# Kernel tuning notes

Measured on AMD Instinct MI355X. Metric: run time of the kernel, lower is better.

The kernel has to match this reference:

```python
import jax, jax.numpy as jnp
import numpy as np

B, T, H, NH = 16, 2048, 1024, 16
HD = H // NH  # 64
IN0, IN1 = 256, 512  # modality input sizes needing projection; modality 2 is already H


def _ln(x, g, b, eps=1e-5):
    m = jnp.mean(x, axis=-1, keepdims=True)
    v = jnp.mean((x - m) ** 2, axis=-1, keepdims=True)
    return (x - m) / jnp.sqrt(v + eps) * g + b


def setup_inputs() -> dict:
    key = jax.random.key(0)
    ks = jax.random.split(key, 24)
    s = 0.02
    d = {
        'x0': jax.random.normal(ks[0], (B, T, IN0), jnp.float32),
        'x1': jax.random.normal(ks[1], (B, T, IN1), jnp.float32),
        'x2': jax.random.normal(ks[2], (B, T, H), jnp.float32),
        'static_context': jax.random.normal(ks[3], (B, T, H), jnp.float32),
        'Wp0': jax.random.normal(ks[4], (H, IN0), jnp.float32) * s,
        'bp0': jnp.zeros((H,), jnp.float32),
        'Wp1': jax.random.normal(ks[5], (H, IN1), jnp.float32) * s,
        'bp1': jnp.zeros((H,), jnp.float32),
        'Wq': jax.random.normal(ks[6], (H, H), jnp.float32) * s,
        'bq': jnp.zeros((H,), jnp.float32),
        'Wk': jax.random.normal(ks[7], (H, H), jnp.float32) * s,
        'bk': jnp.zeros((H,), jnp.float32),
        'Wv': jax.random.normal(ks[8], (H, H), jnp.float32) * s,
        'bv': jnp.zeros((H,), jnp.float32),
        'Wo': jax.random.normal(ks[9], (H, H), jnp.float32) * s,
        'bo': jnp.zeros((H,), jnp.float32),
        'query_token': jax.random.normal(ks[10], (H,), jnp.float32) * s,
        'g1': jnp.ones((H,), jnp.float32),
        'be1': jnp.zeros((H,), jnp.float32),
        'g2': jnp.ones((H,), jnp.float32),
        'be2': jnp.zeros((H,), jnp.float32),
        'W1': jax.random.normal(ks[11], (4 * H, H), jnp.float32) * s,
        'b1': jnp.zeros((4 * H,), jnp.float32),
        'W2': jax.random.normal(ks[12], (H, 4 * H), jnp.float32) * s,
        'b2': jnp.zeros((H,), jnp.float32),
    }
    return d


def _forward(x0, x1, x2, static_context, Wp0, bp0, Wp1, bp1, Wq, bq, Wk, bk, Wv, bv,
             Wo, bo, query_token, g1, be1, g2, be2, W1, b1, W2, b2):
    # project modalities to hidden size, stack -> [B, T, M, H]
    m0 = x0 @ Wp0.T + bp0
    m1 = x1 @ Wp1.T + bp1
    stacked = jnp.stack([m0, m1, x2], axis=2)  # [B,T,3,H]
    M = stacked.shape[2]
    # per-timestep single-query cross-attention over the M modality tokens,
    # batched over all B*T positions (equivalent to the torch per-t loop)
    q = query_token + static_context  # [B,T,H]
    Q = (q @ Wq.T + bq).reshape(B, T, NH, HD)
    K = (stacked @ Wk.T + bk).reshape(B, T, M, NH, HD)
    V = (stacked @ Wv.T + bv).reshape(B, T, M, NH, HD)
    scores = jnp.einsum('bthd,btmhd->bthm', Q, K) / jnp.sqrt(jnp.asarray(HD, Q.dtype))
    attn = jax.nn.softmax(scores, axis=-1)  # [B,T,NH,M]
    weights = attn.mean(axis=2)  # average over heads (torch default) -> [B,T,M]
    ctx = jnp.einsum('bthm,btmhd->bthd', attn, V).reshape(B, T, H)
    attn_out = ctx @ Wo.T + bo
    fused = _ln(attn_out, g1, be1)
    ff = jax.nn.gelu(fused @ W1.T + b1, approximate=False) @ W2.T + b2
    fused = _ln(fused + ff, g2, be2)
    return fused, weights


def reference(x0, x1, x2, static_context, Wp0, bp0, Wp1, bp1, Wq, bq, Wk, bk, Wv, bv,
              Wo, bo, query_token, g1, be1, g2, be2, W1, b1, W2, b2):
    return _forward(x0, x1, x2, static_context, Wp0, bp0, Wp1, bp1, Wq, bq, Wk, bk,
                    Wv, bv, Wo, bo, query_token, g1, be1, g2, be2, W1, b1, W2, b2)
```

## Files before the change

### kernel.cpp

```cpp
#include <hip/hip_runtime.h>
#include <hip/hip_bf16.h>
#include <math.h>

#define BT 32768
#define HH 1024

typedef unsigned short u16;
typedef __attribute__((ext_vector_type(4))) unsigned short u16x4;
typedef __attribute__((ext_vector_type(8))) unsigned short u16x8;
typedef __attribute__((ext_vector_type(8))) __bf16 bf16x8;
typedef __attribute__((ext_vector_type(4))) float f32x4;

#define DEVI static __device__ __forceinline__

DEVI u16 f2bf(float f){
  unsigned u = __builtin_bit_cast(unsigned, f);
  u += 0x7FFFu + ((u >> 16) & 1u);
  return (u16)(u >> 16);
}
DEVI float bf2f(u16 h){
  unsigned u = ((unsigned)h) << 16;
  return __builtin_bit_cast(float, u);
}
DEVI void gl_lds16(const void* g, void* l){
  __builtin_amdgcn_global_load_lds((const __attribute__((address_space(1))) void*)g,
                                   (__attribute__((address_space(3))) void*)l, 16, 0, 0);
}
DEVI int swz(int row, int elem){ return elem ^ ((row & 7) << 3); }

__global__ void k_cast4(const float* __restrict__ s, u16* __restrict__ d, int n4){
  int i = blockIdx.x*blockDim.x + threadIdx.x;
  int st = gridDim.x*blockDim.x;
  for (; i < n4; i += st){
    float4 v = ((const float4*)s)[i];
    u16x4 o = { f2bf(v.x), f2bf(v.y), f2bf(v.z), f2bf(v.w) };
    ((u16x4*)d)[i] = o;
  }
}

__global__ void k_qb(const float* __restrict__ qt, const float* __restrict__ sc,
                     u16* __restrict__ d, int n4){
  int i = blockIdx.x*blockDim.x + threadIdx.x;
  int st = gridDim.x*blockDim.x;
  for (; i < n4; i += st){
    int e = i*4; int c = e & 1023;
    float4 v = *(const float4*)&sc[e];
    float4 q = *(const float4*)&qt[c];
    u16x4 o = { f2bf(v.x+q.x), f2bf(v.y+q.y), f2bf(v.z+q.z), f2bf(v.w+q.w) };
    ((u16x4*)d)[i] = o;
  }
}

__global__ void k_copyf(const float* __restrict__ s, float* __restrict__ d, int n){
  int i = blockIdx.x*blockDim.x + threadIdx.x;
  int st = gridDim.x*blockDim.x;
  for (; i < n; i += st) d[i] = s[i];
}

__global__ void k_wmean(const float* __restrict__ p, float* __restrict__ out, int n){
  int i = blockIdx.x*blockDim.x + threadIdx.x;
  int st = gridDim.x*blockDim.x;
  for (; i < n; i += st){
    int t = i/3, m = i - t*3;
    float s = 0.f;
    #pragma unroll
    for (int h = 0; h < 16; ++h) s += p[(size_t)t*48 + h*3 + m];
    out[i] = s * 0.0625f;
  }
}

__global__ void k_transcast(const float* __restrict__ s, u16* __restrict__ d, int R, int C){
  __shared__ float tile[32][33];
  int c0 = blockIdx.x*32, r0 = blockIdx.y*32;
  int tx = threadIdx.x & 31, ty = threadIdx.x >> 5;
  #pragma unroll
  for (int i = 0; i < 32; i += 8) tile[ty+i][tx] = s[(size_t)(r0+ty+i)*C + c0+tx];
  __syncthreads();
  #pragma unroll
  for (int i = 0; i < 32; i += 8) d[(size_t)(c0+ty+i)*R + r0+tx] = f2bf(tile[tx][ty+i]);
}

__global__ void k_matvec(const u16* __restrict__ W, const float* __restrict__ x,
                         const float* __restrict__ badd, float* __restrict__ out, int K){
  int row = blockIdx.x*4 + (threadIdx.x>>6);
  int lane = threadIdx.x & 63;
  float s = 0.f;
  for (int k = lane; k < K; k += 64) s += bf2f(W[(size_t)row*K + k]) * x[k];
  #pragma unroll
  for (int m = 1; m < 64; m <<= 1) s += __shfl_xor(s, m);
  if (lane == 0) out[row] = s + badd[row];
}

__global__ __launch_bounds__(256, 3)
void k_gemm(const u16* __restrict__ A, int lda,
            const u16* __restrict__ B, int ldb, int K,
            const float* __restrict__ bias,
            u16* __restrict__ C, int ldc, int col0, int act)
{
  __shared__ u16 As[128*64];
  __shared__ u16 Bs[128*64];
  const int tid = threadIdx.x, lane = tid & 63, wid = tid >> 6;
  const int wr = wid >> 1, wc = wid & 1;
  const int r15 = lane & 15, g = lane >> 4;
  const int m0 = blockIdx.x * 128, n0 = blockIdx.y * 128;
  f32x4 acc[4][4] = {};

  for (int k0 = 0; k0 < K; k0 += 64){
    #pragma unroll
    for (int it = 0; it < 4; ++it){
      int c = it*256 + tid;
      int row = c >> 3;
      int ke = swz(row, (c & 7) * 8);
      gl_lds16(A + (size_t)(m0+row)*lda + (k0+ke), As + c*8);
      gl_lds16(B + (size_t)(n0+row)*ldb + (k0+ke), Bs + c*8);
    }
    __syncthreads();
    #pragma unroll
    for (int kk = 0; kk < 64; kk += 32){
      bf16x8 av[4], bvv[4];
      #pragma unroll
      for (int i = 0; i < 4; ++i){
        int row = wr*64 + i*16 + r15;
        av[i] = *(const bf16x8*)&As[row*64 + swz(row, kk + g*8)];
      }
      #pragma unroll
      for (int j = 0; j < 4; ++j){
        int row = wc*64 + j*16 + r15;
        bvv[j] = *(const bf16x8*)&Bs[row*64 + swz(row, kk + g*8)];
      }
      #pragma unroll
      for (int i = 0; i < 4; ++i)
        #pragma unroll
        for (int j = 0; j < 4; ++j)
          acc[i][j] = __builtin_amdgcn_mfma_f32_16x16x32_bf16(av[i], bvv[j], acc[i][j], 0, 0, 0);
    }
    __syncthreads();
  }
  #pragma unroll
  for (int j = 0; j < 4; ++j){
    int col = wc*64 + j*16 + r15;
    float bb = bias ? bias[n0 + col] : 0.f;
    #pragma unroll
    for (int i = 0; i < 4; ++i){
      #pragma unroll
      for (int jj = 0; jj < 4; ++jj){
        int row = wr*64 + i*16 + g*4 + jj;
        float v = acc[i][j][jj] + bb;
        if (act == 1) v = 0.5f * v * (1.f + erff(v * 0.70710678118654752f));
        C[(size_t)(m0+row)*ldc + col0 + n0 + col] = f2bf(v);
      }
    }
  }
}

__global__ __launch_bounds__(256, 2)
void k_attnf(const u16* __restrict__ x0b, const u16* __restrict__ x1b, const u16* __restrict__ x2b,
             const u16* __restrict__ Wc0, const u16* __restrict__ Wc1, const u16* __restrict__ Wc2,
             const float* __restrict__ bc0, const float* __restrict__ bc1, const float* __restrict__ bc2,
             const u16* __restrict__ Qg, u16* __restrict__ ctx, float* __restrict__ pbuf)
{
  __shared__ u16 As[128*64];
  __shared__ u16 Bs[128*64];
  __shared__ float Sl[2*128*3];
  const int tid = threadIdx.x, lane = tid & 63, wid = tid >> 6;
  const int wr = wid >> 1, wc = wid & 1;
  const int r15 = lane & 15, g = lane >> 4;
  const int bid = blockIdx.x;
  const int xcd = bid & 7, bn = (bid >> 3) & 7, btb = (bid >> 6) * 8 + xcd;
  const int t0 = btb * 128, n0 = bn * 128;

  const u16* Xs[3] = { x0b, x1b, x2b };
  const u16* Ws[3] = { Wc0, Wc1, Wc2 };
  const float* Bc[3] = { bc0, bc1, bc2 };
  const int Ks[3] = { 256, 512, 1024 };

  float qreg[4][4][4];
  #pragma unroll
  for (int i = 0; i < 4; ++i)
    #pragma unroll
    for (int jj = 0; jj < 4; ++jj){
      int row = wr*64 + i*16 + g*4 + jj;
      const u16* qr = Qg + (size_t)(t0+row)*1024 + n0 + wc*64 + r15;
      #pragma unroll
      for (int j = 0; j < 4; ++j) qreg[i][jj][j] = bf2f(qr[j*16]);
    }

  #pragma unroll
  for (int m = 0; m < 3; ++m){
    const int K = Ks[m];
    const u16* X = Xs[m];
    const u16* W = Ws[m];
    f32x4 acc[4][4] = {};
    for (int k0 = 0; k0 < K; k0 += 64){
      #pragma unroll
      for (int it = 0; it < 4; ++it){
        int c = it*256 + tid;
        int row = c >> 3;
        int ke = swz(row, (c & 7) * 8);
        gl_lds16(X + (size_t)(t0+row)*K + (k0+ke), As + c*8);
        gl_lds16(W + (size_t)(n0+row)*K + (k0+ke), Bs + c*8);
      }
      __syncthreads();
      #pragma unroll
      for (int kk = 0; kk < 64; kk += 32){
        bf16x8 av[4], bvv[4];
        #pragma unroll
        for (int i = 0; i < 4; ++i){
          int row = wr*64 + i*16 + r15;
          av[i] = *(const bf16x8*)&As[row*64 + swz(row, kk + g*8)];
        }
        #pragma unroll
        for (int j = 0; j < 4; ++j){
          int row = wc*64 + j*16 + r15;
          bvv[j] = *(const bf16x8*)&Bs[row*64 + swz(row, kk + g*8)];
        }
        #pragma unroll
        for (int i = 0; i < 4; ++i)
          #pragma unroll
          for (int j = 0; j < 4; ++j)
            acc[i][j] = __builtin_amdgcn_mfma_f32_16x16x32_bf16(av[i], bvv[j], acc[i][j], 0, 0, 0);
      }
      __syncthreads();
    }
    float bkc[4];
    #pragma unroll
    for (int j = 0; j < 4; ++j) bkc[j] = Bc[m][n0 + wc*64 + j*16 + r15];
    #pragma unroll
    for (int i = 0; i < 4; ++i){
      #pragma unroll
      for (int jj = 0; jj < 4; ++jj){
        int row = wr*64 + i*16 + g*4 + jj;
        float sv = 0.f;
        #pragma unroll
        for (int j = 0; j < 4; ++j)
          sv += (acc[i][j][jj] + bkc[j]) * qreg[i][jj][j];
        sv += __shfl_xor(sv, 1); sv += __shfl_xor(sv, 2);
        sv += __shfl_xor(sv, 4); sv += __shfl_xor(sv, 8);
        if (r15 == 0) Sl[(wc*128 + row)*3 + m] = sv * 0.125f;
      }
    }
  }
  __syncthreads();

  {
    int h2 = tid >> 7, tt = tid & 127;
    int base = (h2*128 + tt)*3;
    float s0 = Sl[base+0], s1 = Sl[base+1], s2 = Sl[base+2];
    float mx = fmaxf(s0, fmaxf(s1, s2));
    float e0 = __expf(s0-mx), e1 = __expf(s1-mx), e2 = __expf(s2-mx);
    float inv = 1.f/(e0+e1+e2);
    e0 *= inv; e1 *= inv; e2 *= inv;
    __syncthreads();
    Sl[base+0] = e0; Sl[base+1] = e1; Sl[base+2] = e2;
    float* pp = pbuf + ((size_t)(t0+tt)*16 + (bn*2 + h2))*3;
    pp[0] = e0; pp[1] = e1; pp[2] = e2;
  }
  __syncthreads();

  f32x4 cx[4][4] = {};
  #pragma unroll
  for (int m = 0; m < 3; ++m){
    const int K = Ks[m];
    const u16* X = Xs[m];
    const u16* W = Ws[m] + (size_t)1024*K;
    f32x4 acc[4][4] = {};
    for (int k0 = 0; k0 < K; k0 += 64){
      #pragma unroll
      for (int it = 0; it < 4; ++it){
        int c = it*256 + tid;
        int row = c >> 3;
        int ke = swz(row, (c & 7) * 8);
        gl_lds16(X + (size_t)(t0+row)*K + (k0+ke), As + c*8);
        gl_lds16(W + (size_t)(n0+row)*K + (k0+ke), Bs + c*8);
      }
      __syncthreads();
      #pragma unroll
      for (int kk = 0; kk < 64; kk += 32){
        bf16x8 av[4], bvv[4];
        #pragma unroll
        for (int i = 0; i < 4; ++i){
          int row = wr*64 + i*16 + r15;
          av[i] = *(const bf16x8*)&As[row*64 + swz(row, kk + g*8)];
        }
        #pragma unroll
        for (int j = 0; j < 4; ++j){
          int row = wc*64 + j*16 + r15;
          bvv[j] = *(const bf16x8*)&Bs[row*64 + swz(row, kk + g*8)];
        }
        #pragma unroll
        for (int i = 0; i < 4; ++i)
          #pragma unroll
          for (int j = 0; j < 4; ++j)
            acc[i][j] = __builtin_amdgcn_mfma_f32_16x16x32_bf16(av[i], bvv[j], acc[i][j], 0, 0, 0);
      }
      __syncthreads();
    }
    float bvc[4];
    #pragma unroll
    for (int j = 0; j < 4; ++j) bvc[j] = Bc[m][1024 + n0 + wc*64 + j*16 + r15];
    #pragma unroll
    for (int i = 0; i < 4; ++i){
      #pragma unroll
      for (int jj = 0; jj < 4; ++jj){
        int row = wr*64 + i*16 + g*4 + jj;
        float p = Sl[(wc*128 + row)*3 + m];
        #pragma unroll
        for (int j = 0; j < 4; ++j)
          cx[i][j][jj] += p * (acc[i][j][jj] + bvc[j]);
      }
    }
  }
  #pragma unroll
  for (int i = 0; i < 4; ++i){
    #pragma unroll
    for (int jj = 0; jj < 4; ++jj){
      int row = wr*64 + i*16 + g*4 + jj;
      #pragma unroll
      for (int j = 0; j < 4; ++j)
        ctx[(size_t)(t0+row)*1024 + n0 + wc*64 + j*16 + r15] = f2bf(cx[i][j][jj]);
    }
  }
}

__global__ __launch_bounds__(256)
void k_ln(const u16* __restrict__ X, const u16* __restrict__ R,
          const float* __restrict__ gam, const float* __restrict__ bet,
          u16* __restrict__ outb, float* __restrict__ outf)
{
  __shared__ float rs[4], rq[4];
  const int t = blockIdx.x, tid = threadIdx.x;
  const size_t base = (size_t)t*1024 + tid*4;
  u16x4 xv = *(const u16x4*)&X[base];
  float v[4];
  #pragma unroll
  for (int i = 0; i < 4; ++i) v[i] = bf2f(xv[i]);
  if (R){
    u16x4 rv = *(const u16x4*)&R[base];
    #pragma unroll
    for (int i = 0; i < 4; ++i) v[i] += bf2f(rv[i]);
  }
  float s = v[0]+v[1]+v[2]+v[3];
  float q = v[0]*v[0]+v[1]*v[1]+v[2]*v[2]+v[3]*v[3];
  #pragma unroll
  for (int m = 1; m < 64; m <<= 1){ s += __shfl_xor(s, m); q += __shfl_xor(q, m); }
  if ((tid & 63) == 0){ rs[tid>>6] = s; rq[tid>>6] = q; }
  __syncthreads();
  s = rs[0]+rs[1]+rs[2]+rs[3];
  q = rq[0]+rq[1]+rq[2]+rq[3];
  float mean = s * (1.f/1024.f);
  float var  = q * (1.f/1024.f) - mean*mean;
  float rstd = rsqrtf(var + 1e-5f);
  int c0 = tid*4;
  if (outb){
    u16x4 o;
    #pragma unroll
    for (int i = 0; i < 4; ++i) o[i] = f2bf((v[i]-mean)*rstd*gam[c0+i] + bet[c0+i]);
    *(u16x4*)&outb[base] = o;
  } else {
    float4 o;
    o.x = (v[0]-mean)*rstd*gam[c0+0] + bet[c0+0];
    o.y = (v[1]-mean)*rstd*gam[c0+1] + bet[c0+1];
    o.z = (v[2]-mean)*rstd*gam[c0+2] + bet[c0+2];
    o.w = (v[3]-mean)*rstd*gam[c0+3] + bet[c0+3];
    *(float4*)&outf[base] = o;
  }
}

extern "C" void kernel_launch(void* const* d_in, const int* in_sizes, int n_in,
                              void* d_out, int out_size, void* d_ws, size_t ws_size,
                              hipStream_t stream)
{
  (void)in_sizes; (void)n_in; (void)out_size;
  const float* x0  = (const float*)d_in[0];
  const float* x1  = (const float*)d_in[1];
  const float* x2  = (const float*)d_in[2];
  const float* sc  = (const float*)d_in[3];
  const float* Wp0 = (const float*)d_in[4];  const float* bp0 = (const float*)d_in[5];
  const float* Wp1 = (const float*)d_in[6];  const float* bp1 = (const float*)d_in[7];
  const float* Wq  = (const float*)d_in[8];  const float* bq  = (const float*)d_in[9];
  const float* Wk  = (const float*)d_in[10]; const float* bk  = (const float*)d_in[11];
  const float* Wv  = (const float*)d_in[12]; const float* bv  = (const float*)d_in[13];
  const float* Wo  = (const float*)d_in[14]; const float* bo  = (const float*)d_in[15];
  const float* qt  = (const float*)d_in[16];
  const float* g1  = (const float*)d_in[17]; const float* be1 = (const float*)d_in[18];
  const float* g2  = (const float*)d_in[19]; const float* be2 = (const float*)d_in[20];
  const float* W1  = (const float*)d_in[21]; const float* b1  = (const float*)d_in[22];
  const float* W2  = (const float*)d_in[23]; const float* b2  = (const float*)d_in[24];

  char* ws = (char*)d_ws;
  size_t off = 0;
  auto alloc = [&](size_t b)->char*{ char* p = ws + off; off += (b + 255) & ~(size_t)255; return p; };

  u16* Wqb   = (u16*)alloc((size_t)1024*1024*2);
  u16* Wob   = (u16*)alloc((size_t)1024*1024*2);
  u16* W1b   = (u16*)alloc((size_t)4096*1024*2);
  u16* W2b   = (u16*)alloc((size_t)1024*4096*2);
  u16* Wkvb  = (u16*)alloc((size_t)2048*1024*2);
  u16* Wp0t  = (u16*)alloc((size_t)256*1024*2);
  u16* Wp1t  = (u16*)alloc((size_t)512*1024*2);
  u16* Wkv0c = (u16*)alloc((size_t)2048*256*2);
  u16* Wkv1c = (u16*)alloc((size_t)2048*512*2);
  float* bc0 = (float*)alloc((size_t)2048*4);
  float* bc1 = (float*)alloc((size_t)2048*4);
  float* bc2 = (float*)alloc((size_t)2048*4);
  char* regX  = alloc((size_t)BT*(256+512+1024)*2);
  char* regQ1 = alloc((size_t)BT*1024*2);
  char* regQ2 = alloc((size_t)BT*1024*2);
  float* pbuf = (float*)alloc((size_t)BT*48*4);
  if (off > ws_size) return;

  u16* x0b = (u16*)regX;
  u16* x1b = (u16*)(regX + (size_t)BT*256*2);
  u16* x2b = (u16*)(regX + (size_t)BT*768*2);
  u16* aob  = (u16*)regX;
  u16* ff2b = (u16*)regX;
  u16* qb   = (u16*)regQ1;
  u16* ctxb = (u16*)regQ1;
  u16* f1b  = (u16*)regQ1;
  u16* Qb   = (u16*)regQ2;
  u16* ff1c = (u16*)regQ2;

  dim3 B256(256);
  auto cast4 = [&](const float* s, u16* d, int n, int grid){
    k_cast4<<<dim3(grid), B256, 0, stream>>>(s, d, n >> 2);
  };
  cast4(Wq, Wqb, 1024*1024, 1024);
  cast4(Wk, Wkvb, 1024*1024, 1024);
  cast4(Wv, Wkvb + (size_t)1024*1024, 1024*1024, 1024);
  cast4(Wo, Wob, 1024*1024, 1024);
  cast4(W1, W1b, 4096*1024, 1024);
  cast4(W2, W2b, 4096*1024, 1024);
  cast4(x0, x0b, BT*256, 1024);
  cast4(x1, x1b, BT*512, 1024);
  cast4(x2, x2b, BT*1024, 2048);
  k_transcast<<<dim3(8, 32),  B256, 0, stream>>>(Wp0, Wp0t, 1024, 256);
  k_transcast<<<dim3(16, 32), B256, 0, stream>>>(Wp1, Wp1t, 1024, 512);
  k_copyf<<<dim3(4), B256, 0, stream>>>(bk, bc2, 1024);
  k_copyf<<<dim3(4), B256, 0, stream>>>(bv, bc2 + 1024, 1024);
  k_matvec<<<dim3(512), B256, 0, stream>>>(Wkvb, bp0, bc2, bc0, 1024);
  k_matvec<<<dim3(512), B256, 0, stream>>>(Wkvb, bp1, bc2, bc1, 1024);
  k_qb<<<dim3(2048), B256, 0, stream>>>(qt, sc, qb, BT*256);

  k_gemm<<<dim3(16, 2), B256, 0, stream>>>(Wkvb, 1024, Wp0t, 1024, 1024, nullptr, Wkv0c, 256, 0, 0);
  k_gemm<<<dim3(16, 4), B256, 0, stream>>>(Wkvb, 1024, Wp1t, 1024, 1024, nullptr, Wkv1c, 512, 0, 0);

  k_gemm<<<dim3(BT/128, 8), B256, 0, stream>>>(qb, 1024, Wqb, 1024, 1024, bq, Qb, 1024, 0, 0);
  k_attnf<<<dim3(BT/128*8), B256, 0, stream>>>(x0b, x1b, x2b, Wkv0c, Wkv1c, Wkvb,
                                               bc0, bc1, bc2, Qb, ctxb, pbuf);
  float* outf = (float*)d_out;
  k_wmean<<<dim3(384), B256, 0, stream>>>(pbuf, outf + (size_t)BT*1024, BT*3);
  k_gemm<<<dim3(BT/128, 8), B256, 0, stream>>>(ctxb, 1024, Wob, 1024, 1024, bo, aob, 1024, 0, 0);
  k_ln<<<dim3(BT), B256, 0, stream>>>(aob, nullptr, g1, be1, f1b, nullptr);

  for (int c = 0; c < 4; ++c){
    const u16* fa = f1b + (size_t)c*8192*1024;
    k_gemm<<<dim3(64, 32), B256, 0, stream>>>(fa, 1024, W1b, 1024, 1024, b1, ff1c, 4096, 0, 1);
    k_gemm<<<dim3(64, 8),  B256, 0, stream>>>(ff1c, 4096, W2b, 4096, 4096, b2,
                                              ff2b + (size_t)c*8192*1024, 1024, 0, 0);
  }
  k_ln<<<dim3(BT), B256, 0, stream>>>(ff2b, f1b, g2, be2, nullptr, outf);
}
```

Baseline: 1.549 ms.

## Cut register pressure in fused attention kernel to raise occupancy

The Q values are no longer held in 64 registers per thread; they are staged through LDS after each K projection. The separate per-modality context accumulator is removed: a single V accumulator is rescaled by ratios of the softmax probabilities between modalities, and biases are applied at the end. Together these free registers, and the launch bound goes from 2 to 3 blocks per SIMD. The risks are extra LDS traffic and barriers, and the probability ratios need a floor clamp to avoid dividing by zero, which changes the rounding behaviour.

```diff
diff --git a/kernel.cpp b/kernel.cpp
--- a/kernel.cpp
+++ b/kernel.cpp
@@ -6,6 +6,7 @@
 #define HH 1024
 
 typedef unsigned short u16;
+typedef unsigned int u32;
 typedef __attribute__((ext_vector_type(4))) unsigned short u16x4;
 typedef __attribute__((ext_vector_type(8))) unsigned short u16x8;
 typedef __attribute__((ext_vector_type(8))) __bf16 bf16x8;
@@ -153,7 +154,7 @@
   }
 }
 
-__global__ __launch_bounds__(256, 2)
+__global__ __launch_bounds__(256, 3)
 void k_attnf(const u16* __restrict__ x0b, const u16* __restrict__ x1b, const u16* __restrict__ x2b,
              const u16* __restrict__ Wc0, const u16* __restrict__ Wc1, const u16* __restrict__ Wc2,
              const float* __restrict__ bc0, const float* __restrict__ bc1, const float* __restrict__ bc2,
@@ -174,17 +175,6 @@
   const float* Bc[3] = { bc0, bc1, bc2 };
   const int Ks[3] = { 256, 512, 1024 };
 
-  float qreg[4][4][4];
-  #pragma unroll
-  for (int i = 0; i < 4; ++i)
-    #pragma unroll
-    for (int jj = 0; jj < 4; ++jj){
-      int row = wr*64 + i*16 + g*4 + jj;
-      const u16* qr = Qg + (size_t)(t0+row)*1024 + n0 + wc*64 + r15;
-      #pragma unroll
-      for (int j = 0; j < 4; ++j) qreg[i][jj][j] = bf2f(qr[j*16]);
-    }
-
   #pragma unroll
   for (int m = 0; m < 3; ++m){
     const int K = Ks[m];
@@ -222,6 +212,16 @@
       }
       __syncthreads();
     }
+    #pragma unroll
+    for (int it = 0; it < 4; ++it){
+      int c = it*256 + tid;
+      int row = c >> 3;
+      int ke = swz(row, (c & 7) * 8);
+      gl_lds16(Qg + (size_t)(t0+row)*1024 + n0 + ke,      As + c*8);
+      gl_lds16(Qg + (size_t)(t0+row)*1024 + n0 + 64 + ke, Bs + c*8);
+    }
+    __syncthreads();
+    const u16* QL = wc ? Bs : As;
     float bkc[4];
     #pragma unroll
     for (int j = 0; j < 4; ++j) bkc[j] = Bc[m][n0 + wc*64 + j*16 + r15];
@@ -233,14 +233,14 @@
         float sv = 0.f;
         #pragma unroll
         for (int j = 0; j < 4; ++j)
-          sv += (acc[i][j][jj] + bkc[j]) * qreg[i][jj][j];
+          sv += (acc[i][j][jj] + bkc[j]) * bf2f(QL[row*64 + swz(row, j*16 + r15)]);
         sv += __shfl_xor(sv, 1); sv += __shfl_xor(sv, 2);
         sv += __shfl_xor(sv, 4); sv += __shfl_xor(sv, 8);
         if (r15 == 0) Sl[(wc*128 + row)*3 + m] = sv * 0.125f;
       }
     }
-  }
-  __syncthreads();
+    __syncthreads();
+  }
 
   {
     int h2 = tid >> 7, tt = tid & 127;
@@ -249,7 +249,7 @@
     float mx = fmaxf(s0, fmaxf(s1, s2));
     float e0 = __expf(s0-mx), e1 = __expf(s1-mx), e2 = __expf(s2-mx);
     float inv = 1.f/(e0+e1+e2);
-    e0 *= inv; e1 *= inv; e2 *= inv;
+    e0 = fmaxf(e0*inv, 1e-30f); e1 = fmaxf(e1*inv, 1e-30f); e2 = fmaxf(e2*inv, 1e-30f);
     __syncthreads();
     Sl[base+0] = e0; Sl[base+1] = e1; Sl[base+2] = e2;
     float* pp = pbuf + ((size_t)(t0+tt)*16 + (bn*2 + h2))*3;
@@ -257,67 +257,77 @@
   }
   __syncthreads();
 
-  f32x4 cx[4][4] = {};
-  #pragma unroll
-  for (int m = 0; m < 3; ++m){
-    const int K = Ks[m];
-    const u16* X = Xs[m];
-    const u16* W = Ws[m] + (size_t)1024*K;
+  {
     f32x4 acc[4][4] = {};
-    for (int k0 = 0; k0 < K; k0 += 64){
-      #pragma unroll
-      for (int it = 0; it < 4; ++it){
-        int c = it*256 + tid;
-        int row = c >> 3;
-        int ke = swz(row, (c & 7) * 8);
-        gl_lds16(X + (size_t)(t0+row)*K + (k0+ke), As + c*8);
-        gl_lds16(W + (size_t)(n0+row)*K + (k0+ke), Bs + c*8);
-      }
-      __syncthreads();
-      #pragma unroll
-      for (int kk = 0; kk < 64; kk += 32){
-        bf16x8 av[4], bvv[4];
+    #pragma unroll
+    for (int m = 0; m < 3; ++m){
+      const int K = Ks[m];
+      const u16* X = Xs[m];
+      const u16* W = Ws[m] + (size_t)1024*K;
+      if (m > 0){
         #pragma unroll
         for (int i = 0; i < 4; ++i){
-          int row = wr*64 + i*16 + r15;
-          av[i] = *(const bf16x8*)&As[row*64 + swz(row, kk + g*8)];
-        }
-        #pragma unroll
-        for (int j = 0; j < 4; ++j){
-          int row = wc*64 + j*16 + r15;
-          bvv[j] = *(const bf16x8*)&Bs[row*64 + swz(row, kk + g*8)];
-        }
-        #pragma unroll
-        for (int i = 0; i < 4; ++i)
           #pragma unroll
-          for (int j = 0; j < 4; ++j)
-            acc[i][j] = __builtin_amdgcn_mfma_f32_16x16x32_bf16(av[i], bvv[j], acc[i][j], 0, 0, 0);
-      }
-      __syncthreads();
-    }
-    float bvc[4];
-    #pragma unroll
-    for (int j = 0; j < 4; ++j) bvc[j] = Bc[m][1024 + n0 + wc*64 + j*16 + r15];
+          for (int jj = 0; jj < 4; ++jj){
+            int row = wr*64 + i*16 + g*4 + jj;
+            float r = Sl[(wc*128+row)*3 + (m-1)] / Sl[(wc*128+row)*3 + m];
+            #pragma unroll
+            for (int j = 0; j < 4; ++j) acc[i][j][jj] *= r;
+          }
+        }
+      }
+      for (int k0 = 0; k0 < K; k0 += 64){
+        #pragma unroll
+        for (int it = 0; it < 4; ++it){
+          int c = it*256 + tid;
+          int row = c >> 3;
+          int ke = swz(row, (c & 7) * 8);
+          gl_lds16(X + (size_t)(t0+row)*K + (k0+ke), As + c*8);
+          gl_lds16(W + (size_t)(n0+row)*K + (k0+ke), Bs + c*8);
+        }
+        __syncthreads();
+        #pragma unroll
+        for (int kk = 0; kk < 64; kk += 32){
+          bf16x8 av[4], bvv[4];
+          #pragma unroll
+          for (int i = 0; i < 4; ++i){
+            int row = wr*64 + i*16 + r15;
+            av[i] = *(const bf16x8*)&As[row*64 + swz(row, kk + g*8)];
+          }
+          #pragma unroll
+          for (int j = 0; j < 4; ++j){
+            int row = wc*64 + j*16 + r15;
+            bvv[j] = *(const bf16x8*)&Bs[row*64 + swz(row, kk + g*8)];
+          }
+          #pragma unroll
+          for (int i = 0; i < 4; ++i)
+            #pragma unroll
+            for (int j = 0; j < 4; ++j)
+              acc[i][j] = __builtin_amdgcn_mfma_f32_16x16x32_bf16(av[i], bvv[j], acc[i][j], 0, 0, 0);
+        }
+        __syncthreads();
+      }
+    }
+    float bvc[3][4];
+    #pragma unroll
+    for (int m = 0; m < 3; ++m)
+      #pragma unroll
+      for (int j = 0; j < 4; ++j)
+        bvc[m][j] = Bc[m][1024 + n0 + wc*64 + j*16 + r15];
     #pragma unroll
     for (int i = 0; i < 4; ++i){
       #pragma unroll
       for (int jj = 0; jj < 4; ++jj){
         int row = wr*64 + i*16 + g*4 + jj;
-        float p = Sl[(wc*128 + row)*3 + m];
-        #pragma unroll
-        for (int j = 0; j < 4; ++j)
-          cx[i][j][jj] += p * (acc[i][j][jj] + bvc[j]);
-      }
-    }
-  }
-  #pragma unroll
-  for (int i = 0; i < 4; ++i){
-    #pragma unroll
-    for (int jj = 0; jj < 4; ++jj){
-      int row = wr*64 + i*16 + g*4 + jj;
-      #pragma unroll
-      for (int j = 0; j < 4; ++j)
-        ctx[(size_t)(t0+row)*1024 + n0 + wc*64 + j*16 + r15] = f2bf(cx[i][j][jj]);
+        float p0 = Sl[(wc*128+row)*3 + 0];
+        float p1 = Sl[(wc*128+row)*3 + 1];
+        float p2 = Sl[(wc*128+row)*3 + 2];
+        #pragma unroll
+        for (int j = 0; j < 4; ++j){
+          float v = acc[i][j][jj]*p2 + p0*bvc[0][j] + p1*bvc[1][j] + p2*bvc[2][j];
+          ctx[(size_t)(t0+row)*1024 + n0 + wc*64 + j*16 + r15] = f2bf(v);
+        }
+      }
     }
   }
 }
```

Result: slower. 1.627 ms (+5.0%).
